# Optimization experiments

Hardware: AMD Instinct MI355X
Metric: run time of the kernel (lower is better)

The kernel has to match this reference:

```python
import jax, jax.numpy as jnp
import numpy as np

B, S, H = 64, 2048, 1024
NEG = -1e10


def setup_inputs() -> dict:
    key = jax.random.key(0)
    k1, k2, k3, k4, k5, k6 = jax.random.split(key, 6)
    scale = 1.0 / np.sqrt(2 * H)
    return {
        "decoder_hidden": jax.random.normal(k1, (B, H), dtype=jnp.float32),
        "encoder_outputs": jax.random.normal(k2, (B, S, H), dtype=jnp.float32),
        "mask": jax.random.randint(k3, (B, S), 0, 2, dtype=jnp.int32),
        "W_attn": jax.random.normal(k4, (2 * H, H), dtype=jnp.float32) * scale,
        "b_attn": jax.random.normal(k5, (H,), dtype=jnp.float32) * scale,
        "v_w": jax.random.normal(k6, (H,), dtype=jnp.float32) * (1.0 / np.sqrt(H)),
    }


def reference(decoder_hidden, encoder_outputs, mask, W_attn, b_attn, v_w):
    # concat((dec_rep, enc), -1) @ W_attn == dec @ W_attn[:H] + enc @ W_attn[H:]
    Wd, We = W_attn[:H], W_attn[H:]
    dec_proj = decoder_hidden @ Wd            # [B, H]
    enc_proj = jnp.einsum('bsh,hk->bsk', encoder_outputs, We)  # [B, S, H]
    energy = jnp.tanh(dec_proj[:, None, :] + enc_proj + b_attn)  # [B, S, H]
    attention = jnp.einsum('bsh,h->bs', energy, v_w)             # [B, S]
    attention = jnp.where(mask == 1, NEG, attention)
    return jax.nn.softmax(attention, axis=1)
```

## Files before the change

### kernel.cpp

```cpp
#include <hip/hip_runtime.h>
#include <hip/hip_bf16.h>
#include <stdint.h>

#define HD   1024
#define BB   64
#define SS   2048
#define MT   (BB*SS)
#define NEGV -10000000000.0f

typedef __attribute__((ext_vector_type(8))) short bf16x8;
typedef __attribute__((ext_vector_type(4))) float f32x4;
typedef __attribute__((ext_vector_type(4))) int   i32x4;

__device__ __forceinline__ void gll16(const void* g, void* l) {
  __builtin_amdgcn_global_load_lds((const __attribute__((address_space(1))) void*)g,
                                   (__attribute__((address_space(3))) void*)l, 16, 0, 0);
}

__device__ __forceinline__ float tanh_fast(float x) {
  float e = __expf(2.0f * x);
  return 1.0f - 2.0f * __builtin_amdgcn_rcpf(e + 1.0f);
}


__global__ void __launch_bounds__(256) prep_all(
    int nE,
    const float* __restrict__ enc, __hip_bfloat16* __restrict__ ebf,
    const float* __restrict__ Wattn, __hip_bfloat16* __restrict__ wet,
    const float* __restrict__ dec, const float* __restrict__ battn,
    float* __restrict__ dpb, float* __restrict__ logits) {
  __shared__ float red[4][64];
  int tid = threadIdx.x;
  int bid = blockIdx.x;

  if (bid < nE) {
    int mt = bid >> 4;
    int l_base = (bid & 15) * 8;
    const float* src = enc + ((size_t)bid * 8) * HD;
    #pragma unroll
    for (int i = 0; i < 4; ++i) {
      int unit = i*256 + tid;
      int r = unit >> 7;
      int j128 = unit & 127;
      int kc = j128 >> 3, jj = j128 & 7;
      int l = l_base + r;
      int jd = jj ^ (l & 7);
      const float* p = src + (size_t)r*HD + j128*8;
      f32x4 v0 = *(const f32x4*)p;
      f32x4 v1 = *(const f32x4*)(p + 4);
      union { __hip_bfloat162 h[4]; i32x4 q; } cv;
      cv.h[0] = __float22bfloat162_rn(make_float2(v0.x, v0.y));
      cv.h[1] = __float22bfloat162_rn(make_float2(v0.z, v0.w));
      cv.h[2] = __float22bfloat162_rn(make_float2(v1.x, v1.y));
      cv.h[3] = __float22bfloat162_rn(make_float2(v1.z, v1.w));
      *(i32x4*)(ebf + ((size_t)(mt*16 + kc))*8192 + l*64 + jd*8) = cv.q;
    }
    return;
  }
  bid -= nE;

  if (bid < 128) {
    int nt = bid >> 4, kc = bid & 15;
    const float* src = Wattn + (size_t)(HD + kc*64)*HD + nt*128;
    size_t base = (size_t)bid * 8192;
    #pragma unroll 4
    for (int i = 0; i < 32; ++i) {
      int lin = i*256 + tid;
      int nl = lin >> 6, j = (lin >> 3) & 7, e = lin & 7;
      int kk = ((j ^ (nl & 7)) << 3) + e;
      wet[base + lin] = __float2bfloat16(src[(size_t)kk*HD + nl]);
    }
    return;
  }
  bid -= 128;

  if (bid < 1024) {
    int b = bid >> 4, n0 = (bid & 15) * 64;
    int nn = tid & 63, kg = tid >> 6;
    const float* wp = Wattn + (size_t)(kg*256)*HD + n0 + nn;
    const float* dp = dec + b*HD + kg*256;
    float acc = 0.0f;
    #pragma unroll 8
    for (int h = 0; h < 256; ++h) acc += dp[h] * wp[(size_t)h*HD];
    red[kg][nn] = acc;
    __syncthreads();
    if (tid < 64) {
      int n = n0 + tid;
      dpb[b*HD + n] = battn[n] + red[0][tid] + red[1][tid]
                               + red[2][tid] + red[3][tid];
    }
    return;
  }
  bid -= 1024;

  f32x4 z = {0.f, 0.f, 0.f, 0.f};
  *(f32x4*)(logits + (size_t)bid*1024 + tid*4) = z;
}

__global__ void __launch_bounds__(512, 2) gemm_fused_8ph(
    const __hip_bfloat16* __restrict__ At, const __hip_bfloat16* __restrict__ Wt,
    const float* __restrict__ dpb, const float* __restrict__ vw,
    float* __restrict__ logits) {
  __shared__ __align__(16) char lds[131072];

  int tid = threadIdx.x;
  int lane = tid & 63, wid = tid >> 6;
  int wm = wid & 1, wn = wid >> 1;
  int lane15 = lane & 15, kg = lane >> 4;

  int x = blockIdx.x & 7, r = blockIdx.x >> 3;
  int bm = x*64 + (r >> 2);
  int bn = r & 3;

  f32x4 acc[2][2][4][2];
  #pragma unroll
  for (int i = 0; i < 2; ++i)
    #pragma unroll
    for (int j = 0; j < 2; ++j)
      #pragma unroll
      for (int k = 0; k < 4; ++k)
        #pragma unroll
        for (int l = 0; l < 2; ++l)
          acc[i][j][k][l] = (f32x4){0.f, 0.f, 0.f, 0.f};

  bf16x8 af[4][2], bfr[2][2];

  auto stage = [&](int op, int h, int t) {
    const char* g = op ? ((const char*)Wt + (((size_t)(bn*2 + h)*16 + t) << 14))
                       : ((const char*)At + (((size_t)(bm*2 + h)*16 + t) << 14));
    char* l = lds + ((t & 1) << 16) + (op << 15) + (h << 14);
    gll16(g + (size_t)(wid*64 + lane)*16,     l + wid*1024);
    gll16(g + (size_t)((8+wid)*64 + lane)*16, l + (8+wid)*1024);
  };
  auto readA = [&](int hr, int t) {
    const char* b = lds + ((t & 1) << 16) + (hr << 14);
    #pragma unroll
    for (int mf = 0; mf < 4; ++mf) {
      int ll = wm*64 + mf*16 + lane15;
      const char* rp = b + ll*128;
      int sw = (ll & 7) << 4;
      af[mf][0] = *(const bf16x8*)(rp + ((kg << 4) ^ sw));
      af[mf][1] = *(const bf16x8*)(rp + (((4 + kg) << 4) ^ sw));
    }
  };
  auto readB = [&](int hc, int t) {
    const char* b = lds + ((t & 1) << 16) + 32768 + (hc << 14);
    #pragma unroll
    for (int nf = 0; nf < 2; ++nf) {
      int ll = wn*32 + nf*16 + lane15;
      const char* rp = b + ll*128;
      int sw = (ll & 7) << 4;
      bfr[nf][0] = *(const bf16x8*)(rp + ((kg << 4) ^ sw));
      bfr[nf][1] = *(const bf16x8*)(rp + (((4 + kg) << 4) ^ sw));
    }
  };

#define MFMA_PH(HR, HC) do {                                                   \
    __builtin_amdgcn_s_setprio(1);                                             \
    _Pragma("unroll")                                                          \
    for (int kk = 0; kk < 2; ++kk)                                             \
      _Pragma("unroll")                                                        \
      for (int mf = 0; mf < 4; ++mf)                                           \
        _Pragma("unroll")                                                      \
        for (int nf = 0; nf < 2; ++nf)                                         \
          acc[HR][HC][mf][nf] = __builtin_amdgcn_mfma_f32_16x16x32_bf16(       \
              af[mf][kk], bfr[nf][kk], acc[HR][HC][mf][nf], 0, 0, 0);          \
    __builtin_amdgcn_s_setprio(0);                                             \
    __builtin_amdgcn_sched_barrier(0);                                         \
  } while (0)

#define PH_SYNC() do {                                                         \
    __builtin_amdgcn_s_barrier();                                              \
    asm volatile("s_waitcnt lgkmcnt(0)");                                      \
    __builtin_amdgcn_sched_barrier(0);                                         \
  } while (0)

  stage(0, 0, 0); stage(1, 1, 0); stage(0, 1, 0); stage(1, 0, 0);
  stage(0, 0, 1); stage(1, 1, 1); stage(0, 1, 1);
  asm volatile("s_waitcnt vmcnt(6)" ::: "memory");
  __builtin_amdgcn_s_barrier();

  #pragma unroll 2
  for (int t = 0; t < 16; ++t) {
    readA(0, t); readB(0, t);
    if (t + 1 < 16) stage(1, 0, t + 1);
    asm volatile("s_waitcnt lgkmcnt(8)");
    PH_SYNC();
    MFMA_PH(0, 0);
    __builtin_amdgcn_s_barrier();

    readB(1, t);
    if (t + 2 < 16) stage(0, 0, t + 2);
    PH_SYNC();
    MFMA_PH(0, 1);
    __builtin_amdgcn_s_barrier();

    readA(1, t);
    if (t + 2 < 16) stage(1, 1, t + 2);
    PH_SYNC();
    MFMA_PH(1, 1);
    __builtin_amdgcn_s_barrier();

    readB(0, t);
    if (t + 2 < 16) stage(0, 1, t + 2);
    PH_SYNC();
    MFMA_PH(1, 0);
    if (t < 14) asm volatile("s_waitcnt vmcnt(6)" ::: "memory");
    else        asm volatile("s_waitcnt vmcnt(0)" ::: "memory");
    __builtin_amdgcn_s_barrier();
  }
#undef MFMA_PH
#undef PH_SYNC

  __syncthreads();
  float* red = (float*)lds;
  if (tid < 256) red[tid] = 0.0f;
  __syncthreads();

  int m0 = bm << 8, n0 = bn << 8;
  int bidx = m0 >> 11;
  float dpv[2][2], vwv[2][2];
  #pragma unroll
  for (int hc = 0; hc < 2; ++hc)
    #pragma unroll
    for (int nf = 0; nf < 2; ++nf) {
      int n = n0 + hc*128 + wn*32 + nf*16 + lane15;
      dpv[hc][nf] = dpb[bidx*HD + n];
      vwv[hc][nf] = vw[n];
    }

  #pragma unroll
  for (int hr = 0; hr < 2; ++hr)
    #pragma unroll
    for (int mf = 0; mf < 4; ++mf)
      #pragma unroll
      for (int rr = 0; rr < 4; ++rr) {
        float s = 0.0f;
        #pragma unroll
        for (int hc = 0; hc < 2; ++hc)
          #pragma unroll
          for (int nf = 0; nf < 2; ++nf)
            s += tanh_fast(acc[hr][hc][mf][nf][rr] + dpv[hc][nf]) * vwv[hc][nf];
        s += __shfl_xor(s, 1); s += __shfl_xor(s, 2);
        s += __shfl_xor(s, 4); s += __shfl_xor(s, 8);
        if (lane15 == 0) atomicAdd(&red[hr*128 + wm*64 + mf*16 + kg*4 + rr], s);
      }
  __syncthreads();
  if (tid < 256) atomicAdd(&logits[m0 + tid], red[tid]);
}

__device__ __forceinline__ void decode_bid(int bid, int& bm, int& bn) {
  int x = bid & 7, r = bid >> 3;
  bm = x*128 + (r >> 3);
  bn = r & 7;
}

__global__ void __launch_bounds__(256) gemm_fused_f32(
    const float* __restrict__ E, const __hip_bfloat16* __restrict__ Wt,
    const float* __restrict__ dpb, const float* __restrict__ vw,
    float* __restrict__ logits) {
  __shared__ __align__(16) short Al[128*72];
  __shared__ __align__(16) short Bl[128*64];
  __shared__ float red[128];

  int tid = threadIdx.x;
  int lane = tid & 63, wid = tid >> 6;
  int wm = wid & 1, wn = wid >> 1;
  int bm, bn; decode_bid(blockIdx.x, bm, bn);
  int m0 = bm << 7, n0 = bn << 7;
  int lane15 = lane & 15, kg = lane >> 4;

  f32x4 acc[4][4];
  #pragma unroll
  for (int a = 0; a < 4; ++a)
    #pragma unroll
    for (int c = 0; c < 4; ++c) acc[a][c] = (f32x4){0.f, 0.f, 0.f, 0.f};

  for (int kc = 0; kc < 16; ++kc) {
    const char* bt = (const char*)Wt + ((size_t)(bn*16 + kc) * 8192) * 2;
    #pragma unroll
    for (int i = 0; i < 4; ++i) {
      int segbase = (wid*4 + i) * 64;
      gll16(bt + (size_t)(segbase + lane)*16, (char*)Bl + segbase*16);
    }
    const float* Eg = E + (m0*HD + kc*64);
    #pragma unroll
    for (int i = 0; i < 8; ++i) {
      int s = i*256 + tid;
      int r = s >> 4, q = s & 15;
      f32x4 v = *(const f32x4*)(Eg + r*HD + q*4);
      union { __hip_bfloat162 h[2]; unsigned long long u; } cv;
      cv.h[0] = __float22bfloat162_rn(make_float2(v.x, v.y));
      cv.h[1] = __float22bfloat162_rn(make_float2(v.z, v.w));
      *(unsigned long long*)&Al[r*72 + q*4] = cv.u;
    }
    __syncthreads();
    #pragma unroll
    for (int kh = 0; kh < 2; ++kh) {
      bf16x8 af[4], bfr[4];
      #pragma unroll
      for (int mf = 0; mf < 4; ++mf) {
        int row = wm*64 + mf*16 + lane15;
        af[mf] = *(const bf16x8*)&Al[row*72 + kh*32 + kg*8];
      }
      #pragma unroll
      for (int nf = 0; nf < 4; ++nf) {
        int nl = wn*64 + nf*16 + lane15;
        int jj = kh*4 + kg;
        bfr[nf] = *(const bf16x8*)&Bl[nl*64 + ((jj ^ (nl & 7)) << 3)];
      }
      #pragma unroll
      for (int mf = 0; mf < 4; ++mf)
        #pragma unroll
        for (int nf = 0; nf < 4; ++nf)
          acc[mf][nf] = __builtin_amdgcn_mfma_f32_16x16x32_bf16(af[mf], bfr[nf], acc[mf][nf], 0, 0, 0);
    }
    __syncthreads();
  }

  int bidx = m0 >> 11;
  float dpv[4], vwv[4];
  #pragma unroll
  for (int nf = 0; nf < 4; ++nf) {
    int n = n0 + wn*64 + nf*16 + lane15;
    dpv[nf] = dpb[bidx*HD + n];
    vwv[nf] = vw[n];
  }
  if (tid < 128) red[tid] = 0.0f;
  __syncthreads();
  #pragma unroll
  for (int mf = 0; mf < 4; ++mf) {
    #pragma unroll
    for (int r = 0; r < 4; ++r) {
      float s = 0.0f;
      #pragma unroll
      for (int nf = 0; nf < 4; ++nf) {
        float x = acc[mf][nf][r] + dpv[nf];
        s += tanh_fast(x) * vwv[nf];
      }
      s += __shfl_xor(s, 1); s += __shfl_xor(s, 2);
      s += __shfl_xor(s, 4); s += __shfl_xor(s, 8);
      if (lane15 == 0) atomicAdd(&red[wm*64 + mf*16 + kg*4 + r], s);
    }
  }
  __syncthreads();
  if (tid < 128) atomicAdd(&logits[m0 + tid], red[tid]);
}

__global__ void softmax_k(const float* __restrict__ logits, const int* __restrict__ mask,
                          float* __restrict__ out) {
  __shared__ float smax[4];
  __shared__ float ssum[4];
  int tid = threadIdx.x, lane = tid & 63, wid = tid >> 6;
  int b = blockIdx.x;
  const float* lg = logits + b*SS;
  const int*   mk = mask   + b*SS;
  f32x4 l0 = *(const f32x4*)(lg + tid*8);
  f32x4 l1 = *(const f32x4*)(lg + tid*8 + 4);
  i32x4 q0 = *(const i32x4*)(mk + tid*8);
  i32x4 q1 = *(const i32x4*)(mk + tid*8 + 4);
  float v[8];
  v[0] = (q0.x == 1) ? NEGV : l0.x;  v[1] = (q0.y == 1) ? NEGV : l0.y;
  v[2] = (q0.z == 1) ? NEGV : l0.z;  v[3] = (q0.w == 1) ? NEGV : l0.w;
  v[4] = (q1.x == 1) ? NEGV : l1.x;  v[5] = (q1.y == 1) ? NEGV : l1.y;
  v[6] = (q1.z == 1) ? NEGV : l1.z;  v[7] = (q1.w == 1) ? NEGV : l1.w;
  float mx = v[0];
  #pragma unroll
  for (int i = 1; i < 8; ++i) mx = fmaxf(mx, v[i]);
  #pragma unroll
  for (int m = 1; m <= 32; m <<= 1) mx = fmaxf(mx, __shfl_xor(mx, m));
  if (lane == 0) smax[wid] = mx;
  __syncthreads();
  mx = fmaxf(fmaxf(smax[0], smax[1]), fmaxf(smax[2], smax[3]));
  float s = 0.0f;
  #pragma unroll
  for (int i = 0; i < 8; ++i) { v[i] = __expf(v[i] - mx); s += v[i]; }
  #pragma unroll
  for (int m = 1; m <= 32; m <<= 1) s += __shfl_xor(s, m);
  if (lane == 0) ssum[wid] = s;
  __syncthreads();
  s = ssum[0] + ssum[1] + ssum[2] + ssum[3];
  float inv = 1.0f / s;
  f32x4 o0 = {v[0]*inv, v[1]*inv, v[2]*inv, v[3]*inv};
  f32x4 o1 = {v[4]*inv, v[5]*inv, v[6]*inv, v[7]*inv};
  *(f32x4*)(out + b*SS + tid*8)     = o0;
  *(f32x4*)(out + b*SS + tid*8 + 4) = o1;
}

extern "C" void kernel_launch(void* const* d_in, const int* in_sizes, int n_in,
                              void* d_out, int out_size, void* d_ws, size_t ws_size,
                              hipStream_t stream) {
  const float* dec   = (const float*)d_in[0];
  const float* enc   = (const float*)d_in[1];
  const int*   mask  = (const int*)  d_in[2];
  const float* Wattn = (const float*)d_in[3];
  const float* battn = (const float*)d_in[4];
  const float* vw    = (const float*)d_in[5];
  float* out = (float*)d_out;

  const size_t EBF_BYTES = (size_t)MT * HD * 2;
  const size_t FAST_NEED = EBF_BYTES + (2u<<20) + (256u<<10) + (512u<<10);

  char* ws = (char*)d_ws;
  if (ws_size >= FAST_NEED) {
    __hip_bfloat16* ebf = (__hip_bfloat16*)ws;
    __hip_bfloat16* wet = (__hip_bfloat16*)(ws + EBF_BYTES);
    float* dpb    = (float*)(ws + EBF_BYTES + (2u<<20));
    float* logits = (float*)(ws + EBF_BYTES + (2u<<20) + (256u<<10));

    prep_all<<<16384 + 1280, 256, 0, stream>>>(16384, enc, ebf, Wattn, wet,
                                               dec, battn, dpb, logits);
    gemm_fused_8ph<<<2048, 512, 0, stream>>>(ebf, wet, dpb, vw, logits);
    softmax_k<<<BB, 256, 0, stream>>>(logits, mask, out);
  } else {
    __hip_bfloat16* wet = (__hip_bfloat16*)ws;
    float* dpb    = (float*)(ws + (2u<<20));
    float* logits = (float*)(ws + (2u<<20) + (256u<<10));

    prep_all<<<1280, 256, 0, stream>>>(0, nullptr, nullptr, Wattn, wet,
                                       dec, battn, dpb, logits);
    gemm_fused_f32<<<8192, 256, 0, stream>>>(enc, wet, dpb, vw, logits);
    softmax_k<<<BB, 256, 0, stream>>>(logits, mask, out);
  }
}
```

Before: 1.028 ms.

## Fuse fp32-to-bf16 encoder conversion into GEMM A-tile loading

Drops the separate pass that converted the whole encoder tensor to a swizzled bf16 workspace copy. The main GEMM kernel now loads fp32 encoder rows into registers, converts them to bf16 and writes them into swizzled LDS, software-pipelined two k-steps ahead, while the W tiles still use direct global-to-LDS loads. This removes a full write and re-read of the large bf16 intermediate, at the cost of more register pressure, doubled A-side global traffic per tile (fp32) and conversion ALU work inside the main loop. The fallback fp32 GEMM path is removed.

```diff
diff --git a/kernel.cpp b/kernel.cpp
--- a/kernel.cpp
+++ b/kernel.cpp
@@ -23,41 +23,13 @@
 }
 
 
-__global__ void __launch_bounds__(256) prep_all(
-    int nE,
-    const float* __restrict__ enc, __hip_bfloat16* __restrict__ ebf,
+__global__ void __launch_bounds__(256) prep_small(
     const float* __restrict__ Wattn, __hip_bfloat16* __restrict__ wet,
     const float* __restrict__ dec, const float* __restrict__ battn,
     float* __restrict__ dpb, float* __restrict__ logits) {
   __shared__ float red[4][64];
   int tid = threadIdx.x;
   int bid = blockIdx.x;
-
-  if (bid < nE) {
-    int mt = bid >> 4;
-    int l_base = (bid & 15) * 8;
-    const float* src = enc + ((size_t)bid * 8) * HD;
-    #pragma unroll
-    for (int i = 0; i < 4; ++i) {
-      int unit = i*256 + tid;
-      int r = unit >> 7;
-      int j128 = unit & 127;
-      int kc = j128 >> 3, jj = j128 & 7;
-      int l = l_base + r;
-      int jd = jj ^ (l & 7);
-      const float* p = src + (size_t)r*HD + j128*8;
-      f32x4 v0 = *(const f32x4*)p;
-      f32x4 v1 = *(const f32x4*)(p + 4);
-      union { __hip_bfloat162 h[4]; i32x4 q; } cv;
-      cv.h[0] = __float22bfloat162_rn(make_float2(v0.x, v0.y));
-      cv.h[1] = __float22bfloat162_rn(make_float2(v0.z, v0.w));
-      cv.h[2] = __float22bfloat162_rn(make_float2(v1.x, v1.y));
-      cv.h[3] = __float22bfloat162_rn(make_float2(v1.z, v1.w));
-      *(i32x4*)(ebf + ((size_t)(mt*16 + kc))*8192 + l*64 + jd*8) = cv.q;
-    }
-    return;
-  }
-  bid -= nE;
 
   if (bid < 128) {
     int nt = bid >> 4, kc = bid & 15;
@@ -98,7 +70,7 @@
 }
 
 __global__ void __launch_bounds__(512, 2) gemm_fused_8ph(
-    const __hip_bfloat16* __restrict__ At, const __hip_bfloat16* __restrict__ Wt,
+    const float* __restrict__ enc, const __hip_bfloat16* __restrict__ Wt,
     const float* __restrict__ dpb, const float* __restrict__ vw,
     float* __restrict__ logits) {
   __shared__ __align__(16) char lds[131072];
@@ -111,6 +83,7 @@
   int x = blockIdx.x & 7, r = blockIdx.x >> 3;
   int bm = x*64 + (r >> 2);
   int bn = r & 3;
+  int m0 = bm << 8, n0 = bn << 8;
 
   f32x4 acc[2][2][4][2];
   #pragma unroll
@@ -125,10 +98,51 @@
 
   bf16x8 af[4][2], bfr[2][2];
 
-  auto stage = [&](int op, int h, int t) {
-    const char* g = op ? ((const char*)Wt + (((size_t)(bn*2 + h)*16 + t) << 14))
-                       : ((const char*)At + (((size_t)(bm*2 + h)*16 + t) << 14));
-    char* l = lds + ((t & 1) << 16) + (op << 15) + (h << 14);
+  int rA = tid >> 2, qA = tid & 3;
+  const float* encR0 = enc + ((size_t)(m0 + rA))*HD + qA*16;
+  const float* encR1 = enc + ((size_t)(m0 + 128 + rA))*HD + qA*16;
+  int swA = (rA & 7) << 4;
+  int wo0 = ((qA*2    ) << 4) ^ swA;
+  int wo1 = ((qA*2 + 1) << 4) ^ swA;
+
+  f32x4 aP[8], aQ[8];
+
+  auto loadA = [&](int t2, f32x4 (&d)[8]) {
+    const float* p0 = encR0 + t2*64;
+    const float* p1 = encR1 + t2*64;
+    d[0] = *(const f32x4*)(p0);      d[1] = *(const f32x4*)(p0 + 4);
+    d[2] = *(const f32x4*)(p0 + 8);  d[3] = *(const f32x4*)(p0 + 12);
+    d[4] = *(const f32x4*)(p1);      d[5] = *(const f32x4*)(p1 + 4);
+    d[6] = *(const f32x4*)(p1 + 8);  d[7] = *(const f32x4*)(p1 + 12);
+  };
+  auto writeA = [&](int tw, f32x4 (&s)[8]) {
+    char* b0 = lds + ((tw & 1) << 16) + rA*128;
+    char* b1 = b0 + 16384;
+    union { __hip_bfloat162 h[4]; i32x4 q; } c0, c1, c2, c3;
+    c0.h[0] = __float22bfloat162_rn(make_float2(s[0].x, s[0].y));
+    c0.h[1] = __float22bfloat162_rn(make_float2(s[0].z, s[0].w));
+    c0.h[2] = __float22bfloat162_rn(make_float2(s[1].x, s[1].y));
+    c0.h[3] = __float22bfloat162_rn(make_float2(s[1].z, s[1].w));
+    c1.h[0] = __float22bfloat162_rn(make_float2(s[2].x, s[2].y));
+    c1.h[1] = __float22bfloat162_rn(make_float2(s[2].z, s[2].w));
+    c1.h[2] = __float22bfloat162_rn(make_float2(s[3].x, s[3].y));
+    c1.h[3] = __float22bfloat162_rn(make_float2(s[3].z, s[3].w));
+    c2.h[0] = __float22bfloat162_rn(make_float2(s[4].x, s[4].y));
+    c2.h[1] = __float22bfloat162_rn(make_float2(s[4].z, s[4].w));
+    c2.h[2] = __float22bfloat162_rn(make_float2(s[5].x, s[5].y));
+    c2.h[3] = __float22bfloat162_rn(make_float2(s[5].z, s[5].w));
+    c3.h[0] = __float22bfloat162_rn(make_float2(s[6].x, s[6].y));
+    c3.h[1] = __float22bfloat162_rn(make_float2(s[6].z, s[6].w));
+    c3.h[2] = __float22bfloat162_rn(make_float2(s[7].x, s[7].y));
+    c3.h[3] = __float22bfloat162_rn(make_float2(s[7].z, s[7].w));
+    *(i32x4*)(b0 + wo0) = c0.q;
+    *(i32x4*)(b0 + wo1) = c1.q;
+    *(i32x4*)(b1 + wo0) = c2.q;
+    *(i32x4*)(b1 + wo1) = c3.q;
+  };
+  auto stageB = [&](int h, int t) {
+    const char* g = (const char*)Wt + (((size_t)(bn*2 + h)*16 + t) << 14);
+    char* l = lds + ((t & 1) << 16) + (1 << 15) + (h << 14);
     gll16(g + (size_t)(wid*64 + lane)*16,     l + wid*1024);
     gll16(g + (size_t)((8+wid)*64 + lane)*16, l + (8+wid)*1024);
   };
@@ -175,38 +189,48 @@
     __builtin_amdgcn_sched_barrier(0);                                         \
   } while (0)
 
-  stage(0, 0, 0); stage(1, 1, 0); stage(0, 1, 0); stage(1, 0, 0);
-  stage(0, 0, 1); stage(1, 1, 1); stage(0, 1, 1);
-  asm volatile("s_waitcnt vmcnt(6)" ::: "memory");
+  loadA(0, aP);
+  loadA(1, aQ);
+  stageB(0, 0); stageB(1, 0);
+  asm volatile("s_waitcnt vmcnt(12)" ::: "memory");
+  __builtin_amdgcn_sched_barrier(0);
+  writeA(0, aP);
+  asm volatile("s_waitcnt vmcnt(4)" ::: "memory");
+  __builtin_amdgcn_sched_barrier(0);
+  writeA(1, aQ);
+  asm volatile("s_waitcnt vmcnt(0) lgkmcnt(0)" ::: "memory");
   __builtin_amdgcn_s_barrier();
 
   #pragma unroll 2
   for (int t = 0; t < 16; ++t) {
+    if (t + 1 < 16) { stageB(0, t + 1); stageB(1, t + 1); }
     readA(0, t); readB(0, t);
-    if (t + 1 < 16) stage(1, 0, t + 1);
     asm volatile("s_waitcnt lgkmcnt(8)");
     PH_SYNC();
     MFMA_PH(0, 0);
     __builtin_amdgcn_s_barrier();
 
     readB(1, t);
-    if (t + 2 < 16) stage(0, 0, t + 2);
     PH_SYNC();
     MFMA_PH(0, 1);
     __builtin_amdgcn_s_barrier();
 
     readA(1, t);
-    if (t + 2 < 16) stage(1, 1, t + 2);
+    if (t >= 1 && t + 1 < 16) {
+      asm volatile("s_waitcnt vmcnt(4)" ::: "memory");
+      __builtin_amdgcn_sched_barrier(0);
+      writeA(t + 1, aP);
+    }
     PH_SYNC();
     MFMA_PH(1, 1);
     __builtin_amdgcn_s_barrier();
 
     readB(0, t);
-    if (t + 2 < 16) stage(0, 1, t + 2);
+    if (t + 2 < 16) loadA(t + 2, aP);
     PH_SYNC();
     MFMA_PH(1, 0);
-    if (t < 14) asm volatile("s_waitcnt vmcnt(6)" ::: "memory");
-    else        asm volatile("s_waitcnt vmcnt(0)" ::: "memory");
+    if (t < 14)       asm volatile("s_waitcnt vmcnt(8)" ::: "memory");
+    else if (t == 14) asm volatile("s_waitcnt vmcnt(0)" ::: "memory");
     __builtin_amdgcn_s_barrier();
   }
 #undef MFMA_PH
@@ -217,7 +241,6 @@
   if (tid < 256) red[tid] = 0.0f;
   __syncthreads();
 
-  int m0 = bm << 8, n0 = bn << 8;
   int bidx = m0 >> 11;
   float dpv[2][2], vwv[2][2];
   #pragma unroll
@@ -247,104 +270,6 @@
       }
   __syncthreads();
   if (tid < 256) atomicAdd(&logits[m0 + tid], red[tid]);
-}
-
-__device__ __forceinline__ void decode_bid(int bid, int& bm, int& bn) {
-  int x = bid & 7, r = bid >> 3;
-  bm = x*128 + (r >> 3);
-  bn = r & 7;
-}
-
-__global__ void __launch_bounds__(256) gemm_fused_f32(
-    const float* __restrict__ E, const __hip_bfloat16* __restrict__ Wt,
-    const float* __restrict__ dpb, const float* __restrict__ vw,
-    float* __restrict__ logits) {
-  __shared__ __align__(16) short Al[128*72];
-  __shared__ __align__(16) short Bl[128*64];
-  __shared__ float red[128];
-
-  int tid = threadIdx.x;
-  int lane = tid & 63, wid = tid >> 6;
-  int wm = wid & 1, wn = wid >> 1;
-  int bm, bn; decode_bid(blockIdx.x, bm, bn);
-  int m0 = bm << 7, n0 = bn << 7;
-  int lane15 = lane & 15, kg = lane >> 4;
-
-  f32x4 acc[4][4];
-  #pragma unroll
-  for (int a = 0; a < 4; ++a)
-    #pragma unroll
-    for (int c = 0; c < 4; ++c) acc[a][c] = (f32x4){0.f, 0.f, 0.f, 0.f};
-
-  for (int kc = 0; kc < 16; ++kc) {
-    const char* bt = (const char*)Wt + ((size_t)(bn*16 + kc) * 8192) * 2;
-    #pragma unroll
-    for (int i = 0; i < 4; ++i) {
-      int segbase = (wid*4 + i) * 64;
-      gll16(bt + (size_t)(segbase + lane)*16, (char*)Bl + segbase*16);
-    }
-    const float* Eg = E + (m0*HD + kc*64);
-    #pragma unroll
-    for (int i = 0; i < 8; ++i) {
-      int s = i*256 + tid;
-      int r = s >> 4, q = s & 15;
-      f32x4 v = *(const f32x4*)(Eg + r*HD + q*4);
-      union { __hip_bfloat162 h[2]; unsigned long long u; } cv;
-      cv.h[0] = __float22bfloat162_rn(make_float2(v.x, v.y));
-      cv.h[1] = __float22bfloat162_rn(make_float2(v.z, v.w));
-      *(unsigned long long*)&Al[r*72 + q*4] = cv.u;
-    }
-    __syncthreads();
-    #pragma unroll
-    for (int kh = 0; kh < 2; ++kh) {
-      bf16x8 af[4], bfr[4];
-      #pragma unroll
-      for (int mf = 0; mf < 4; ++mf) {
-        int row = wm*64 + mf*16 + lane15;
-        af[mf] = *(const bf16x8*)&Al[row*72 + kh*32 + kg*8];
-      }
-      #pragma unroll
-      for (int nf = 0; nf < 4; ++nf) {
-        int nl = wn*64 + nf*16 + lane15;
-        int jj = kh*4 + kg;
-        bfr[nf] = *(const bf16x8*)&Bl[nl*64 + ((jj ^ (nl & 7)) << 3)];
-      }
-      #pragma unroll
-      for (int mf = 0; mf < 4; ++mf)
-        #pragma unroll
-        for (int nf = 0; nf < 4; ++nf)
-          acc[mf][nf] = __builtin_amdgcn_mfma_f32_16x16x32_bf16(af[mf], bfr[nf], acc[mf][nf], 0, 0, 0);
-    }
-    __syncthreads();
-  }
-
-  int bidx = m0 >> 11;
-  float dpv[4], vwv[4];
-  #pragma unroll
-  for (int nf = 0; nf < 4; ++nf) {
-    int n = n0 + wn*64 + nf*16 + lane15;
-    dpv[nf] = dpb[bidx*HD + n];
-    vwv[nf] = vw[n];
-  }
-  if (tid < 128) red[tid] = 0.0f;
-  __syncthreads();
-  #pragma unroll
-  for (int mf = 0; mf < 4; ++mf) {
-    #pragma unroll
-    for (int r = 0; r < 4; ++r) {
-      float s = 0.0f;
-      #pragma unroll
-      for (int nf = 0; nf < 4; ++nf) {
-        float x = acc[mf][nf][r] + dpv[nf];
-        s += tanh_fast(x) * vwv[nf];
-      }
-      s += __shfl_xor(s, 1); s += __shfl_xor(s, 2);
-      s += __shfl_xor(s, 4); s += __shfl_xor(s, 8);
-      if (lane15 == 0) atomicAdd(&red[wm*64 + mf*16 + kg*4 + r], s);
-    }
-  }
-  __syncthreads();
-  if (tid < 128) atomicAdd(&logits[m0 + tid], red[tid]);
 }
 
 __global__ void softmax_k(const float* __restrict__ logits, const int* __restrict__ mask,
@@ -398,28 +323,12 @@
   const float* vw    = (const float*)d_in[5];
   float* out = (float*)d_out;
 
-  const size_t EBF_BYTES = (size_t)MT * HD * 2;
-  const size_t FAST_NEED = EBF_BYTES + (2u<<20) + (256u<<10) + (512u<<10);
-
   char* ws = (char*)d_ws;
-  if (ws_size >= FAST_NEED) {
-    __hip_bfloat16* ebf = (__hip_bfloat16*)ws;
-    __hip_bfloat16* wet = (__hip_bfloat16*)(ws + EBF_BYTES);
-    float* dpb    = (float*)(ws + EBF_BYTES + (2u<<20));
-    float* logits = (float*)(ws + EBF_BYTES + (2u<<20) + (256u<<10));
-
-    prep_all<<<16384 + 1280, 256, 0, stream>>>(16384, enc, ebf, Wattn, wet,
-                                               dec, battn, dpb, logits);
-    gemm_fused_8ph<<<2048, 512, 0, stream>>>(ebf, wet, dpb, vw, logits);
-    softmax_k<<<BB, 256, 0, stream>>>(logits, mask, out);
-  } else {
-    __hip_bfloat16* wet = (__hip_bfloat16*)ws;
-    float* dpb    = (float*)(ws + (2u<<20));
-    float* logits = (float*)(ws + (2u<<20) + (256u<<10));
-
-    prep_all<<<1280, 256, 0, stream>>>(0, nullptr, nullptr, Wattn, wet,
-                                       dec, battn, dpb, logits);
-    gemm_fused_f32<<<8192, 256, 0, stream>>>(enc, wet, dpb, vw, logits);
-    softmax_k<<<BB, 256, 0, stream>>>(logits, mask, out);
-  }
-}
+  __hip_bfloat16* wet = (__hip_bfloat16*)ws;
+  float* dpb    = (float*)(ws + (2u<<20));
+  float* logits = (float*)(ws + (2u<<20) + (256u<<10));
+
+  prep_small<<<1280, 256, 0, stream>>>(Wattn, wet, dec, battn, dpb, logits);
+  gemm_fused_8ph<<<2048, 512, 0, stream>>>(enc, wet, dpb, vw, logits);
+  softmax_k<<<BB, 256, 0, stream>>>(logits, mask, out);
+}
```

New measurement: 1.208 ms. +17.5%, slower.
